# Kernel optimization log

Hardware: AMD Instinct MI355X
Metric: run time of the kernel (lower is better)

## Reference

```python
import jax, jax.numpy as jnp
import numpy as np

DIM = 256
NUM_EXPERTS = 16
EXPERT_HIDDEN = 128
ROUTER_HIDDEN = 64
N_TOKENS = 32768


def setup_inputs() -> dict:
    key = jax.random.key(0)
    ks = jax.random.split(key, 9)
    s = lambda fan_in: 1.0 / np.sqrt(fan_in)
    x = jax.random.normal(ks[0], (N_TOKENS, DIM), dtype=jnp.float32)
    # Router params (Linear(DIM,64) -> ReLU -> Linear(64,E))
    r_w1 = jax.random.uniform(ks[1], (DIM, ROUTER_HIDDEN), jnp.float32, -s(DIM), s(DIM))
    r_b1 = jax.random.uniform(ks[2], (ROUTER_HIDDEN,), jnp.float32, -s(DIM), s(DIM))
    r_w2 = jax.random.uniform(ks[3], (ROUTER_HIDDEN, NUM_EXPERTS), jnp.float32, -s(ROUTER_HIDDEN), s(ROUTER_HIDDEN))
    r_b2 = jax.random.uniform(ks[4], (NUM_EXPERTS,), jnp.float32, -s(ROUTER_HIDDEN), s(ROUTER_HIDDEN))
    # Expert params, stacked over experts: Linear(DIM,128) -> Tanh -> Linear(128,DIM)
    e_w1 = jax.random.uniform(ks[5], (NUM_EXPERTS, DIM, EXPERT_HIDDEN), jnp.float32, -s(DIM), s(DIM))
    e_b1 = jax.random.uniform(ks[6], (NUM_EXPERTS, EXPERT_HIDDEN), jnp.float32, -s(DIM), s(DIM))
    e_w2 = jax.random.uniform(ks[7], (NUM_EXPERTS, EXPERT_HIDDEN, DIM), jnp.float32, -s(EXPERT_HIDDEN), s(EXPERT_HIDDEN))
    e_b2 = jax.random.uniform(ks[8], (NUM_EXPERTS, DIM), jnp.float32, -s(EXPERT_HIDDEN), s(EXPERT_HIDDEN))
    return {"x": x, "r_w1": r_w1, "r_b1": r_b1, "r_w2": r_w2, "r_b2": r_b2,
            "e_w1": e_w1, "e_b1": e_b1, "e_w2": e_w2, "e_b2": e_b2}


def reference(x, r_w1, r_b1, r_w2, r_b2, e_w1, e_b1, e_w2, e_b2):
    # Router: softmax(Linear(ReLU(Linear(x)))), temp=1.0
    h_r = jax.nn.relu(x @ r_w1 + r_b1)                      # [N, 64]
    w = jax.nn.softmax(h_r @ r_w2 + r_b2, axis=-1)          # [N, E]
    # All experts densely (faithful to the reference loop), batched over E.
    h = jnp.tanh(jnp.einsum('nd,edh->neh', x, e_w1) + e_b1[None, :, :])   # [N, E, H]
    outs = jnp.einsum('neh,ehd->ned', h, e_w2) + e_b2[None, :, :]         # [N, E, D]
    # Top-2 gating: mask, renormalize, combine.
    top_val, top_idx = jax.lax.top_k(w, 2)                  # [N, 2]
    n = w.shape[0]
    mask = jnp.zeros_like(w).at[jnp.arange(n)[:, None], top_idx].set(1.0)
    w_top = w * mask
    w_top = w_top / (jnp.sum(w_top, axis=-1, keepdims=True) + 1e-8)
    y_pred = jnp.einsum('ne,ned->nd', w_top, outs)          # [N, D]
    return (y_pred, w)
```

## Files before the change

### kernel.cpp

```cpp
#include <hip/hip_runtime.h>
#include <math.h>

#define NT 32768
#define DIM 256
#define NE 16
#define EH 128
#define RH 64
#define TB 64

#define IB (NT * DIM)
#define WS_COUNTS (IB)
#define WS_OFFSETS (IB + 16)
#define WS_CURSORS (IB + 33)
#define WS_NBLK (IB + 49)
#define WS_TABLE (IB + 64)
#define WS_TOKE (IB + 4096)
#define WS_LIST (WS_TOKE + 2 * NT)
#define WS_TOKG (WS_LIST + 2 * NT)
#define WS_LIST_G (WS_TOKG + 2 * NT)
#define WS_END_I (WS_LIST_G + 2 * NT)
#define U_W1T (2 * WS_END_I)
#define U_W2T (U_W1T + NE * DIM * EH)
#define U_XG (U_W2T + NE * DIM * EH)

typedef __attribute__((ext_vector_type(4))) float f32x4;
typedef __attribute__((ext_vector_type(8))) short bf16x8;
typedef __attribute__((ext_vector_type(8))) unsigned short us8;

#define SWZ9(b) ((b) ^ (((b) >> 5) & 0x70))
#define SWZ8(b) ((b) ^ (((b) >> 4) & 0x70))

__device__ inline unsigned short f2bf(float f) {
    unsigned int bits = __builtin_bit_cast(unsigned int, f);
    bits += 0x7fffu + ((bits >> 16) & 1u);
    return (unsigned short)(bits >> 16);
}

__global__ __launch_bounds__(256) void router_kernel(
    const float* __restrict__ x,
    const float* __restrict__ rw1, const float* __restrict__ rb1,
    const float* __restrict__ rw2, const float* __restrict__ rb2,
    float* __restrict__ w_out, int* __restrict__ wsi, float* __restrict__ wsf)
{
    __shared__ float xT[64][68];
    __shared__ float w1s[64][64];
    __shared__ float hs[64][68];
    __shared__ float ls[64][20];
    __shared__ int scnt[16];

    const int tid = threadIdx.x;
    const int tok0 = blockIdx.x * 64;
    if (tid < 16) scnt[tid] = 0;

    float acc[4][4];
#pragma unroll
    for (int i = 0; i < 4; ++i)
#pragma unroll
        for (int j = 0; j < 4; ++j) acc[i][j] = 0.f;

    const int tt = (tid & 15) * 4;
    const int hh = (tid >> 4) * 4;

    for (int kc = 0; kc < 4; ++kc) {
        __syncthreads();
#pragma unroll
        for (int i = 0; i < 4; ++i) {
            int idx = tid + 256 * i;
            int t = idx >> 4;
            int d4 = (idx & 15) * 4;
            float4 v = *(const float4*)(x + (size_t)(tok0 + t) * DIM + kc * 64 + d4);
            xT[d4 + 0][t] = v.x; xT[d4 + 1][t] = v.y;
            xT[d4 + 2][t] = v.z; xT[d4 + 3][t] = v.w;
        }
#pragma unroll
        for (int i = 0; i < 4; ++i) {
            int idx = tid + 256 * i;
            int d = idx >> 4;
            int h4 = (idx & 15) * 4;
            *(float4*)&w1s[d][h4] = *(const float4*)(rw1 + (size_t)(kc * 64 + d) * RH + h4);
        }
        __syncthreads();
#pragma unroll 8
        for (int d = 0; d < 64; ++d) {
            const float4 xa4 = *(const float4*)&xT[d][tt];
            const float4 wv4 = *(const float4*)&w1s[d][hh];
            const float xa[4] = {xa4.x, xa4.y, xa4.z, xa4.w};
            const float wv[4] = {wv4.x, wv4.y, wv4.z, wv4.w};
#pragma unroll
            for (int i = 0; i < 4; ++i)
#pragma unroll
                for (int j = 0; j < 4; ++j)
                    acc[i][j] = fmaf(xa[i], wv[j], acc[i][j]);
        }
    }
    __syncthreads();
    {
        const float4 b4 = *(const float4*)(rb1 + hh);
        const float b[4] = {b4.x, b4.y, b4.z, b4.w};
#pragma unroll
        for (int i = 0; i < 4; ++i) {
            float4 hv;
            hv.x = fmaxf(acc[i][0] + b[0], 0.f);
            hv.y = fmaxf(acc[i][1] + b[1], 0.f);
            hv.z = fmaxf(acc[i][2] + b[2], 0.f);
            hv.w = fmaxf(acc[i][3] + b[3], 0.f);
            *(float4*)&hs[tt + i][hh] = hv;
        }
    }
    __syncthreads();
    {
        int tok = tid >> 2;
        int e0 = (tid & 3) * 4;
        float l[4] = {0.f, 0.f, 0.f, 0.f};
#pragma unroll 8
        for (int k = 0; k < 64; ++k) {
            float hv = hs[tok][k];
            float4 wv = *(const float4*)(rw2 + k * NE + e0);
            l[0] = fmaf(hv, wv.x, l[0]);
            l[1] = fmaf(hv, wv.y, l[1]);
            l[2] = fmaf(hv, wv.z, l[2]);
            l[3] = fmaf(hv, wv.w, l[3]);
        }
        float4 lb = *(const float4*)(rb2 + e0);
        ls[tok][e0 + 0] = l[0] + lb.x;
        ls[tok][e0 + 1] = l[1] + lb.y;
        ls[tok][e0 + 2] = l[2] + lb.z;
        ls[tok][e0 + 3] = l[3] + lb.w;
    }
    __syncthreads();
    if (tid < 64) {
        const int tok = tid;
        const int gt = tok0 + tok;
        float v[16];
        float m = -1e30f;
#pragma unroll
        for (int e = 0; e < 16; ++e) { v[e] = ls[tok][e]; m = fmaxf(m, v[e]); }
        float s = 0.f;
#pragma unroll
        for (int e = 0; e < 16; ++e) { v[e] = expf(v[e] - m); s += v[e]; }
        const float inv = 1.0f / s;
#pragma unroll
        for (int e = 0; e < 16; ++e) v[e] *= inv;
#pragma unroll
        for (int e = 0; e < 16; e += 4) {
            float4 wv = make_float4(v[e], v[e + 1], v[e + 2], v[e + 3]);
            *(float4*)(w_out + (size_t)gt * NE + e) = wv;
        }
        float v1 = -1.f, v2 = -1.f; int i1 = 0, i2 = 0;
#pragma unroll
        for (int e = 0; e < 16; ++e) {
            if (v[e] > v1) { v2 = v1; i2 = i1; v1 = v[e]; i1 = e; }
            else if (v[e] > v2) { v2 = v[e]; i2 = e; }
        }
        const float den = v1 + v2 + 1e-8f;
        atomicAdd(&scnt[i1], 1);
        atomicAdd(&scnt[i2], 1);
        wsi[WS_TOKE + 2 * gt + 0] = i1;
        wsi[WS_TOKE + 2 * gt + 1] = i2;
        wsf[WS_TOKG + 2 * gt + 0] = v1 / den;
        wsf[WS_TOKG + 2 * gt + 1] = v2 / den;
    }
    __syncthreads();
    if (tid < 16 && scnt[tid]) atomicAdd(&wsi[WS_COUNTS + tid], scnt[tid]);
}

__global__ __launch_bounds__(256) void wprep_kernel(
    const float* __restrict__ ew1, const float* __restrict__ ew2,
    unsigned short* __restrict__ w1t, unsigned short* __restrict__ w2t)
{
    __shared__ float t[64][65];
    int b = blockIdx.x;
    const float* src; unsigned short* dst; int R, C, tr, tc;
    if (b < 128) {
        int e = b >> 3, t8 = b & 7; tr = t8 >> 1; tc = t8 & 1;
        src = ew1 + (size_t)e * DIM * EH; R = DIM; C = EH;
        dst = w1t + (size_t)e * DIM * EH;
    } else {
        int b2 = b - 128; int e = b2 >> 3, t8 = b2 & 7; tr = t8 & 1; tc = t8 >> 1;
        src = ew2 + (size_t)e * EH * DIM; R = EH; C = DIM;
        dst = w2t + (size_t)e * EH * DIM;
    }
    const int R0 = tr * 64, C0 = tc * 64;
    const int tid = threadIdx.x;
#pragma unroll
    for (int q = 0; q < 4; ++q) {
        int r = (tid >> 4) + q * 16, c = (tid & 15) * 4;
        float4 v = *(const float4*)(src + (size_t)(R0 + r) * C + C0 + c);
        t[r][c] = v.x; t[r][c + 1] = v.y; t[r][c + 2] = v.z; t[r][c + 3] = v.w;
    }
    __syncthreads();
#pragma unroll
    for (int q = 0; q < 2; ++q) {
        int rp = (tid >> 3) + q * 32, c0 = (tid & 7) * 8;
        us8 u;
#pragma unroll
        for (int k = 0; k < 8; ++k) u[k] = f2bf(t[c0 + k][rp]);
        *(us8*)(dst + (size_t)(C0 + rp) * R + R0 + c0) = u;
    }
}

__global__ __launch_bounds__(64) void scan_kernel(int* __restrict__ wsi)
{
    __shared__ int soff[17], snc[16];
    const int tid = threadIdx.x;
    if (tid == 0) {
        int off = 0, nb = 0;
        soff[0] = 0;
        for (int e = 0; e < NE; ++e) {
            int c = wsi[WS_COUNTS + e];
            wsi[WS_CURSORS + e] = off;
            wsi[WS_OFFSETS + e] = off;
            off += c;
            soff[e + 1] = off;
            snc[e] = nb;
            nb += (c + TB - 1) / TB;
        }
        wsi[WS_OFFSETS + NE] = off;
        wsi[WS_NBLK] = nb;
    }
    __syncthreads();
    for (int e = 0; e < NE; ++e) {
        int nc = (soff[e + 1] - soff[e] + TB - 1) / TB;
        for (int k = tid; k < nc; k += 64)
            wsi[WS_TABLE + snc[e] + k] = (e << 16) | k;
    }
}

__global__ __launch_bounds__(256) void scatter_kernel(int* __restrict__ wsi, float* __restrict__ wsf)
{
    __shared__ int scnt[16], sbase[16];
    const int tid = threadIdx.x;
    const int t = blockIdx.x * 256 + tid;
    if (tid < 16) scnt[tid] = 0;
    __syncthreads();
    const int e0 = wsi[WS_TOKE + 2 * t + 0];
    const int e1 = wsi[WS_TOKE + 2 * t + 1];
    const int l0 = atomicAdd(&scnt[e0], 1);
    const int l1 = atomicAdd(&scnt[e1], 1);
    __syncthreads();
    if (tid < 16) sbase[tid] = scnt[tid] ? atomicAdd(&wsi[WS_CURSORS + tid], scnt[tid]) : 0;
    __syncthreads();
    const int p0 = sbase[e0] + l0;
    const int p1 = sbase[e1] + l1;
    wsi[WS_LIST + p0] = (t << 1);
    wsf[WS_LIST_G + p0] = wsf[WS_TOKG + 2 * t + 0];
    wsi[WS_LIST + p1] = (t << 1) | 1;
    wsf[WS_LIST_G + p1] = wsf[WS_TOKG + 2 * t + 1];
}

__global__ __launch_bounds__(256) void gather_kernel(
    const float* __restrict__ x, const int* __restrict__ wsi,
    unsigned short* __restrict__ xg)
{
    const int tid = threadIdx.x;
    const int p = blockIdx.x * 32 + (tid >> 3);
    const int sub = tid & 7;
    const int tok = wsi[WS_LIST + p] >> 1;
    const float* src = x + (size_t)tok * DIM + sub * 32;
    unsigned short* dst = xg + (size_t)p * DIM + sub * 32;
    float4 v[8];
#pragma unroll
    for (int i = 0; i < 8; ++i) v[i] = *(const float4*)(src + i * 4);
#pragma unroll
    for (int i = 0; i < 4; ++i) {
        us8 u;
        u[0] = f2bf(v[2 * i].x);     u[1] = f2bf(v[2 * i].y);
        u[2] = f2bf(v[2 * i].z);     u[3] = f2bf(v[2 * i].w);
        u[4] = f2bf(v[2 * i + 1].x); u[5] = f2bf(v[2 * i + 1].y);
        u[6] = f2bf(v[2 * i + 1].z); u[7] = f2bf(v[2 * i + 1].w);
        *(us8*)(dst + i * 8) = u;
    }
}

__global__ __launch_bounds__(256, 1) void expert_kernel(
    const unsigned short* __restrict__ xg,
    const float* __restrict__ eb1, const float* __restrict__ eb2,
    const unsigned short* __restrict__ w1t, const unsigned short* __restrict__ w2t,
    const int* __restrict__ wsi, const float* __restrict__ wsf,
    float* __restrict__ y, float* __restrict__ part1)
{
    __shared__ unsigned short smem[16384];
    if ((int)blockIdx.x >= wsi[WS_NBLK]) return;

    const int ent = wsi[WS_TABLE + blockIdx.x];
    const int e = ent >> 16;
    const int c = ent & 0xffff;
    const int start = wsi[WS_OFFSETS + e] + c * TB;
    const int cnt = min(TB, wsi[WS_OFFSETS + e + 1] - start);

    const int tid = threadIdx.x;
    const int lane = tid & 63, w = tid >> 6;
    const int l15 = lane & 15;
    const int kq = lane >> 4;
    const int q4 = kq * 4;
    char* lds = (char*)smem;

    const char* xrow = (const char*)(xg + (size_t)start * DIM);
    us8 ubuf[8];
#pragma unroll
    for (int i = 0; i < 8; ++i)
        ubuf[i] = *(const us8*)(xrow + (tid + i * 256) * 16);

    const char* w1e = (const char*)(w1t + (size_t)e * DIM * EH);
    bf16x8 b1[8][2];
#pragma unroll
    for (int ks = 0; ks < 8; ++ks)
#pragma unroll
        for (int nt = 0; nt < 2; ++nt)
            b1[ks][nt] = *(const bf16x8*)(w1e + (w * 32 + nt * 16 + l15) * 512 + ks * 64 + kq * 16);

#pragma unroll
    for (int i = 0; i < 8; ++i)
        *(us8*)(lds + SWZ9((tid + i * 256) * 16)) = ubuf[i];
    __syncthreads();

    f32x4 zero4; zero4[0] = zero4[1] = zero4[2] = zero4[3] = 0.f;
    f32x4 acc[4][2];
#pragma unroll
    for (int i = 0; i < 4; ++i)
#pragma unroll
        for (int j = 0; j < 2; ++j) acc[i][j] = zero4;

#pragma unroll
    for (int ks = 0; ks < 8; ++ks) {
        bf16x8 a[4];
#pragma unroll
        for (int mt = 0; mt < 4; ++mt)
            a[mt] = *(const bf16x8*)(lds + SWZ9((mt * 16 + l15) * 512 + ks * 64 + kq * 16));
#pragma unroll
        for (int mt = 0; mt < 4; ++mt)
#pragma unroll
            for (int nt = 0; nt < 2; ++nt)
                acc[mt][nt] = __builtin_amdgcn_mfma_f32_16x16x32_bf16(a[mt], b1[ks][nt], acc[mt][nt], 0, 0, 0);
    }

    const char* w2e = (const char*)(w2t + (size_t)e * EH * DIM);
    bf16x8 b2a[4][2];
#pragma unroll
    for (int ks = 0; ks < 4; ++ks)
#pragma unroll
        for (int nt = 0; nt < 2; ++nt)
            b2a[ks][nt] = *(const bf16x8*)(w2e + (w * 64 + nt * 16 + l15) * 256 + ks * 64 + kq * 16);

    __syncthreads();

#pragma unroll
    for (int nt = 0; nt < 2; ++nt) {
        const int h = w * 32 + nt * 16 + l15;
        const float b1v = eb1[e * EH + h];
#pragma unroll
        for (int mt = 0; mt < 4; ++mt)
#pragma unroll
            for (int r = 0; r < 4; ++r) {
                int tok = mt * 16 + q4 + r;
                *(unsigned short*)(lds + SWZ8(tok * 256 + h * 2)) = f2bf(tanhf(acc[mt][nt][r] + b1v));
            }
    }
    __syncthreads();

    bf16x8 b2b[4][2];
#pragma unroll
    for (int ks = 0; ks < 4; ++ks)
#pragma unroll
        for (int nt = 0; nt < 2; ++nt)
            b2b[ks][nt] = *(const bf16x8*)(w2e + (w * 64 + 32 + nt * 16 + l15) * 256 + ks * 64 + kq * 16);

    {
        f32x4 acc2[4][2];
#pragma unroll
        for (int i = 0; i < 4; ++i)
#pragma unroll
            for (int j = 0; j < 2; ++j) acc2[i][j] = zero4;
#pragma unroll
        for (int ks = 0; ks < 4; ++ks) {
            bf16x8 a[4];
#pragma unroll
            for (int mt = 0; mt < 4; ++mt)
                a[mt] = *(const bf16x8*)(lds + SWZ8((mt * 16 + l15) * 256 + ks * 64 + kq * 16));
#pragma unroll
            for (int mt = 0; mt < 4; ++mt)
#pragma unroll
                for (int nt = 0; nt < 2; ++nt)
                    acc2[mt][nt] = __builtin_amdgcn_mfma_f32_16x16x32_bf16(a[mt], b2a[ks][nt], acc2[mt][nt], 0, 0, 0);
        }
        float b2v[2];
#pragma unroll
        for (int nt = 0; nt < 2; ++nt)
            b2v[nt] = eb2[e * DIM + w * 64 + nt * 16 + l15];
#pragma unroll
        for (int mt = 0; mt < 4; ++mt)
#pragma unroll
            for (int r = 0; r < 4; ++r) {
                int rl = mt * 16 + q4 + r;
                if (rl < cnt) {
                    int entry = wsi[WS_LIST + start + rl];
                    int tok = entry >> 1;
                    float g = wsf[WS_LIST_G + start + rl];
                    float* dst = ((entry & 1) ? part1 : y) + (size_t)tok * DIM + w * 64;
#pragma unroll
                    for (int nt = 0; nt < 2; ++nt)
                        dst[nt * 16 + l15] = g * (acc2[mt][nt][r] + b2v[nt]);
                }
            }
    }
    {
        f32x4 acc2[4][2];
#pragma unroll
        for (int i = 0; i < 4; ++i)
#pragma unroll
            for (int j = 0; j < 2; ++j) acc2[i][j] = zero4;
#pragma unroll
        for (int ks = 0; ks < 4; ++ks) {
            bf16x8 a[4];
#pragma unroll
            for (int mt = 0; mt < 4; ++mt)
                a[mt] = *(const bf16x8*)(lds + SWZ8((mt * 16 + l15) * 256 + ks * 64 + kq * 16));
#pragma unroll
            for (int mt = 0; mt < 4; ++mt)
#pragma unroll
                for (int nt = 0; nt < 2; ++nt)
                    acc2[mt][nt] = __builtin_amdgcn_mfma_f32_16x16x32_bf16(a[mt], b2b[ks][nt], acc2[mt][nt], 0, 0, 0);
        }
        float b2v[2];
#pragma unroll
        for (int nt = 0; nt < 2; ++nt)
            b2v[nt] = eb2[e * DIM + w * 64 + 32 + nt * 16 + l15];
#pragma unroll
        for (int mt = 0; mt < 4; ++mt)
#pragma unroll
            for (int r = 0; r < 4; ++r) {
                int rl = mt * 16 + q4 + r;
                if (rl < cnt) {
                    int entry = wsi[WS_LIST + start + rl];
                    int tok = entry >> 1;
                    float g = wsf[WS_LIST_G + start + rl];
                    float* dst = ((entry & 1) ? part1 : y) + (size_t)tok * DIM + w * 64 + 32;
#pragma unroll
                    for (int nt = 0; nt < 2; ++nt)
                        dst[nt * 16 + l15] = g * (acc2[mt][nt][r] + b2v[nt]);
                }
            }
    }
}

__global__ __launch_bounds__(256) void combine_kernel(float* __restrict__ y,
                                                      const float* __restrict__ part1)
{
    const size_t i = ((size_t)blockIdx.x * 256 + threadIdx.x) * 4;
    float4 a = *(float4*)(y + i);
    const float4 b = *(const float4*)(part1 + i);
    a.x += b.x; a.y += b.y; a.z += b.z; a.w += b.w;
    *(float4*)(y + i) = a;
}

extern "C" void kernel_launch(void* const* d_in, const int* in_sizes, int n_in,
                              void* d_out, int out_size, void* d_ws, size_t ws_size,
                              hipStream_t stream)
{
    const float* x = (const float*)d_in[0];
    const float* rw1 = (const float*)d_in[1];
    const float* rb1 = (const float*)d_in[2];
    const float* rw2 = (const float*)d_in[3];
    const float* rb2 = (const float*)d_in[4];
    const float* ew1 = (const float*)d_in[5];
    const float* eb1 = (const float*)d_in[6];
    const float* ew2 = (const float*)d_in[7];
    const float* eb2 = (const float*)d_in[8];

    float* y = (float*)d_out;
    float* w_out = y + (size_t)NT * DIM;
    int* wsi = (int*)d_ws;
    float* wsf = (float*)d_ws;
    float* part1 = (float*)d_ws;
    unsigned short* wsu = (unsigned short*)d_ws;

    hipMemsetAsync(wsi + WS_COUNTS, 0, NE * sizeof(int), stream);

    wprep_kernel<<<256, 256, 0, stream>>>(ew1, ew2, wsu + U_W1T, wsu + U_W2T);
    router_kernel<<<NT / 64, 256, 0, stream>>>(x, rw1, rb1, rw2, rb2, w_out, wsi, wsf);
    scan_kernel<<<1, 64, 0, stream>>>(wsi);
    scatter_kernel<<<NT / 256, 256, 0, stream>>>(wsi, wsf);
    gather_kernel<<<2 * NT / 32, 256, 0, stream>>>(x, wsi, wsu + U_XG);
    expert_kernel<<<2 * NT / TB + NE, 256, 0, stream>>>(wsu + U_XG, eb1, eb2,
                                                        wsu + U_W1T, wsu + U_W2T,
                                                        wsi, wsf, y, part1);
    combine_kernel<<<NT * DIM / 1024, 256, 0, stream>>>(y, part1);
}
```

Before: 137.7 us.

## Make expert kernel persistent with 2 blocks/CU, LDS-cached routing, fast tanh

Turns the expert kernel into a persistent grid of 512 blocks that loop over the block table, instead of launching one block per tile. It raises the launch bound to two blocks per CU, stages each tile's token list and gate values in shared memory once, and replaces tanhf with an exp-based fast tanh. The aim is to cut launch and early-exit overhead, improve latency hiding, and remove repeated global reads of the routing lists. The tradeoff is tighter register pressure and possible spills, plus an extra barrier per tile and small tanh accuracy changes.

```diff
diff --git a/kernel.cpp b/kernel.cpp
--- a/kernel.cpp
+++ b/kernel.cpp
@@ -7,6 +7,7 @@
 #define EH 128
 #define RH 64
 #define TB 64
+#define NPERS 512
 
 #define IB (NT * DIM)
 #define WS_COUNTS (IB)
@@ -36,6 +37,12 @@
     return (unsigned short)(bits >> 16);
 }
 
+__device__ inline float fast_tanh(float v) {
+    float cv = fminf(fmaxf(v, -15.f), 15.f);
+    float ex = __expf(2.f * cv);
+    return (ex - 1.f) / (ex + 1.f);
+}
+
 __global__ __launch_bounds__(256) void router_kernel(
     const float* __restrict__ x,
     const float* __restrict__ rw1, const float* __restrict__ rb1,
@@ -272,7 +279,7 @@
     }
 }
 
-__global__ __launch_bounds__(256, 1) void expert_kernel(
+__global__ __launch_bounds__(256, 2) void expert_kernel(
     const unsigned short* __restrict__ xg,
     const float* __restrict__ eb1, const float* __restrict__ eb2,
     const unsigned short* __restrict__ w1t, const unsigned short* __restrict__ w2t,
@@ -280,166 +287,175 @@
     float* __restrict__ y, float* __restrict__ part1)
 {
     __shared__ unsigned short smem[16384];
-    if ((int)blockIdx.x >= wsi[WS_NBLK]) return;
-
-    const int ent = wsi[WS_TABLE + blockIdx.x];
-    const int e = ent >> 16;
-    const int c = ent & 0xffff;
-    const int start = wsi[WS_OFFSETS + e] + c * TB;
-    const int cnt = min(TB, wsi[WS_OFFSETS + e + 1] - start);
-
+    __shared__ int sl[64];
+    __shared__ float sg[64];
+
+    const int nblk = wsi[WS_NBLK];
     const int tid = threadIdx.x;
     const int lane = tid & 63, w = tid >> 6;
     const int l15 = lane & 15;
     const int kq = lane >> 4;
     const int q4 = kq * 4;
     char* lds = (char*)smem;
-
-    const char* xrow = (const char*)(xg + (size_t)start * DIM);
-    us8 ubuf[8];
-#pragma unroll
-    for (int i = 0; i < 8; ++i)
-        ubuf[i] = *(const us8*)(xrow + (tid + i * 256) * 16);
-
-    const char* w1e = (const char*)(w1t + (size_t)e * DIM * EH);
-    bf16x8 b1[8][2];
-#pragma unroll
-    for (int ks = 0; ks < 8; ++ks)
-#pragma unroll
-        for (int nt = 0; nt < 2; ++nt)
-            b1[ks][nt] = *(const bf16x8*)(w1e + (w * 32 + nt * 16 + l15) * 512 + ks * 64 + kq * 16);
-
-#pragma unroll
-    for (int i = 0; i < 8; ++i)
-        *(us8*)(lds + SWZ9((tid + i * 256) * 16)) = ubuf[i];
-    __syncthreads();
-
     f32x4 zero4; zero4[0] = zero4[1] = zero4[2] = zero4[3] = 0.f;
-    f32x4 acc[4][2];
-#pragma unroll
-    for (int i = 0; i < 4; ++i)
-#pragma unroll
-        for (int j = 0; j < 2; ++j) acc[i][j] = zero4;
-
-#pragma unroll
-    for (int ks = 0; ks < 8; ++ks) {
-        bf16x8 a[4];
-#pragma unroll
-        for (int mt = 0; mt < 4; ++mt)
-            a[mt] = *(const bf16x8*)(lds + SWZ9((mt * 16 + l15) * 512 + ks * 64 + kq * 16));
-#pragma unroll
-        for (int mt = 0; mt < 4; ++mt)
+
+    for (int bi = blockIdx.x; bi < nblk; bi += NPERS) {
+        const int ent = wsi[WS_TABLE + bi];
+        const int e = ent >> 16;
+        const int c = ent & 0xffff;
+        const int start = wsi[WS_OFFSETS + e] + c * TB;
+        const int cnt = min(TB, wsi[WS_OFFSETS + e + 1] - start);
+
+        __syncthreads();
+
+        const char* xrow = (const char*)(xg + (size_t)start * DIM);
+        us8 ubuf[8];
+#pragma unroll
+        for (int i = 0; i < 8; ++i)
+            ubuf[i] = *(const us8*)(xrow + (tid + i * 256) * 16);
+
+        const char* w1e = (const char*)(w1t + (size_t)e * DIM * EH);
+        bf16x8 b1[8][2];
+#pragma unroll
+        for (int ks = 0; ks < 8; ++ks)
 #pragma unroll
             for (int nt = 0; nt < 2; ++nt)
-                acc[mt][nt] = __builtin_amdgcn_mfma_f32_16x16x32_bf16(a[mt], b1[ks][nt], acc[mt][nt], 0, 0, 0);
-    }
-
-    const char* w2e = (const char*)(w2t + (size_t)e * EH * DIM);
-    bf16x8 b2a[4][2];
-#pragma unroll
-    for (int ks = 0; ks < 4; ++ks)
-#pragma unroll
-        for (int nt = 0; nt < 2; ++nt)
-            b2a[ks][nt] = *(const bf16x8*)(w2e + (w * 64 + nt * 16 + l15) * 256 + ks * 64 + kq * 16);
-
-    __syncthreads();
-
-#pragma unroll
-    for (int nt = 0; nt < 2; ++nt) {
-        const int h = w * 32 + nt * 16 + l15;
-        const float b1v = eb1[e * EH + h];
-#pragma unroll
-        for (int mt = 0; mt < 4; ++mt)
-#pragma unroll
-            for (int r = 0; r < 4; ++r) {
-                int tok = mt * 16 + q4 + r;
-                *(unsigned short*)(lds + SWZ8(tok * 256 + h * 2)) = f2bf(tanhf(acc[mt][nt][r] + b1v));
+                b1[ks][nt] = *(const bf16x8*)(w1e + (w * 32 + nt * 16 + l15) * 512 + ks * 64 + kq * 16);
+
+        if (tid < 64) {
+            sl[tid] = (tid < cnt) ? wsi[WS_LIST + start + tid] : 0;
+            sg[tid] = (tid < cnt) ? wsf[WS_LIST_G + start + tid] : 0.f;
+        }
+
+#pragma unroll
+        for (int i = 0; i < 8; ++i)
+            *(us8*)(lds + SWZ9((tid + i * 256) * 16)) = ubuf[i];
+        __syncthreads();
+
+        f32x4 acc[4][2];
+#pragma unroll
+        for (int i = 0; i < 4; ++i)
+#pragma unroll
+            for (int j = 0; j < 2; ++j) acc[i][j] = zero4;
+
+#pragma unroll
+        for (int ks = 0; ks < 8; ++ks) {
+            bf16x8 a[4];
+#pragma unroll
+            for (int mt = 0; mt < 4; ++mt)
+                a[mt] = *(const bf16x8*)(lds + SWZ9((mt * 16 + l15) * 512 + ks * 64 + kq * 16));
+#pragma unroll
+            for (int mt = 0; mt < 4; ++mt)
+#pragma unroll
+                for (int nt = 0; nt < 2; ++nt)
+                    acc[mt][nt] = __builtin_amdgcn_mfma_f32_16x16x32_bf16(a[mt], b1[ks][nt], acc[mt][nt], 0, 0, 0);
+        }
+
+        const char* w2e = (const char*)(w2t + (size_t)e * EH * DIM);
+        bf16x8 b2a[4][2];
+#pragma unroll
+        for (int ks = 0; ks < 4; ++ks)
+#pragma unroll
+            for (int nt = 0; nt < 2; ++nt)
+                b2a[ks][nt] = *(const bf16x8*)(w2e + (w * 64 + nt * 16 + l15) * 256 + ks * 64 + kq * 16);
+
+        __syncthreads();
+
+#pragma unroll
+        for (int nt = 0; nt < 2; ++nt) {
+            const int h = w * 32 + nt * 16 + l15;
+            const float b1v = eb1[e * EH + h];
+#pragma unroll
+            for (int mt = 0; mt < 4; ++mt)
+#pragma unroll
+                for (int r = 0; r < 4; ++r) {
+                    int tok = mt * 16 + q4 + r;
+                    *(unsigned short*)(lds + SWZ8(tok * 256 + h * 2)) = f2bf(fast_tanh(acc[mt][nt][r] + b1v));
+                }
+        }
+        __syncthreads();
+
+        bf16x8 b2b[4][2];
+#pragma unroll
+        for (int ks = 0; ks < 4; ++ks)
+#pragma unroll
+            for (int nt = 0; nt < 2; ++nt)
+                b2b[ks][nt] = *(const bf16x8*)(w2e + (w * 64 + 32 + nt * 16 + l15) * 256 + ks * 64 + kq * 16);
+
+        {
+            f32x4 acc2[4][2];
+#pragma unroll
+            for (int i = 0; i < 4; ++i)
+#pragma unroll
+                for (int j = 0; j < 2; ++j) acc2[i][j] = zero4;
+#pragma unroll
+            for (int ks = 0; ks < 4; ++ks) {
+                bf16x8 a[4];
+#pragma unroll
+                for (int mt = 0; mt < 4; ++mt)
+                    a[mt] = *(const bf16x8*)(lds + SWZ8((mt * 16 + l15) * 256 + ks * 64 + kq * 16));
+#pragma unroll
+                for (int mt = 0; mt < 4; ++mt)
+#pragma unroll
+                    for (int nt = 0; nt < 2; ++nt)
+                        acc2[mt][nt] = __builtin_amdgcn_mfma_f32_16x16x32_bf16(a[mt], b2a[ks][nt], acc2[mt][nt], 0, 0, 0);
             }
-    }
-    __syncthreads();
-
-    bf16x8 b2b[4][2];
-#pragma unroll
-    for (int ks = 0; ks < 4; ++ks)
-#pragma unroll
-        for (int nt = 0; nt < 2; ++nt)
-            b2b[ks][nt] = *(const bf16x8*)(w2e + (w * 64 + 32 + nt * 16 + l15) * 256 + ks * 64 + kq * 16);
-
-    {
-        f32x4 acc2[4][2];
-#pragma unroll
-        for (int i = 0; i < 4; ++i)
-#pragma unroll
-            for (int j = 0; j < 2; ++j) acc2[i][j] = zero4;
-#pragma unroll
-        for (int ks = 0; ks < 4; ++ks) {
-            bf16x8 a[4];
+            float b2v[2];
+#pragma unroll
+            for (int nt = 0; nt < 2; ++nt)
+                b2v[nt] = eb2[e * DIM + w * 64 + nt * 16 + l15];
 #pragma unroll
             for (int mt = 0; mt < 4; ++mt)
-                a[mt] = *(const bf16x8*)(lds + SWZ8((mt * 16 + l15) * 256 + ks * 64 + kq * 16));
+#pragma unroll
+                for (int r = 0; r < 4; ++r) {
+                    int rl = mt * 16 + q4 + r;
+                    if (rl < cnt) {
+                        int entry = sl[rl];
+                        float g = sg[rl];
+                        float* dst = ((entry & 1) ? part1 : y) + (size_t)(entry >> 1) * DIM + w * 64;
+#pragma unroll
+                        for (int nt = 0; nt < 2; ++nt)
+                            dst[nt * 16 + l15] = g * (acc2[mt][nt][r] + b2v[nt]);
+                    }
+                }
+        }
+        {
+            f32x4 acc2[4][2];
+#pragma unroll
+            for (int i = 0; i < 4; ++i)
+#pragma unroll
+                for (int j = 0; j < 2; ++j) acc2[i][j] = zero4;
+#pragma unroll
+            for (int ks = 0; ks < 4; ++ks) {
+                bf16x8 a[4];
+#pragma unroll
+                for (int mt = 0; mt < 4; ++mt)
+                    a[mt] = *(const bf16x8*)(lds + SWZ8((mt * 16 + l15) * 256 + ks * 64 + kq * 16));
+#pragma unroll
+                for (int mt = 0; mt < 4; ++mt)
+#pragma unroll
+                    for (int nt = 0; nt < 2; ++nt)
+                        acc2[mt][nt] = __builtin_amdgcn_mfma_f32_16x16x32_bf16(a[mt], b2b[ks][nt], acc2[mt][nt], 0, 0, 0);
+            }
+            float b2v[2];
+#pragma unroll
+            for (int nt = 0; nt < 2; ++nt)
+                b2v[nt] = eb2[e * DIM + w * 64 + 32 + nt * 16 + l15];
 #pragma unroll
             for (int mt = 0; mt < 4; ++mt)
 #pragma unroll
-                for (int nt = 0; nt < 2; ++nt)
-                    acc2[mt][nt] = __builtin_amdgcn_mfma_f32_16x16x32_bf16(a[mt], b2a[ks][nt], acc2[mt][nt], 0, 0, 0);
-        }
-        float b2v[2];
-#pragma unroll
-        for (int nt = 0; nt < 2; ++nt)
-            b2v[nt] = eb2[e * DIM + w * 64 + nt * 16 + l15];
-#pragma unroll
-        for (int mt = 0; mt < 4; ++mt)
-#pragma unroll
-            for (int r = 0; r < 4; ++r) {
-                int rl = mt * 16 + q4 + r;
-                if (rl < cnt) {
-                    int entry = wsi[WS_LIST + start + rl];
-                    int tok = entry >> 1;
-                    float g = wsf[WS_LIST_G + start + rl];
-                    float* dst = ((entry & 1) ? part1 : y) + (size_t)tok * DIM + w * 64;
-#pragma unroll
-                    for (int nt = 0; nt < 2; ++nt)
-                        dst[nt * 16 + l15] = g * (acc2[mt][nt][r] + b2v[nt]);
+                for (int r = 0; r < 4; ++r) {
+                    int rl = mt * 16 + q4 + r;
+                    if (rl < cnt) {
+                        int entry = sl[rl];
+                        float g = sg[rl];
+                        float* dst = ((entry & 1) ? part1 : y) + (size_t)(entry >> 1) * DIM + w * 64 + 32;
+#pragma unroll
+                        for (int nt = 0; nt < 2; ++nt)
+                            dst[nt * 16 + l15] = g * (acc2[mt][nt][r] + b2v[nt]);
+                    }
                 }
-            }
-    }
-    {
-        f32x4 acc2[4][2];
-#pragma unroll
-        for (int i = 0; i < 4; ++i)
-#pragma unroll
-            for (int j = 0; j < 2; ++j) acc2[i][j] = zero4;
-#pragma unroll
-        for (int ks = 0; ks < 4; ++ks) {
-            bf16x8 a[4];
-#pragma unroll
-            for (int mt = 0; mt < 4; ++mt)
-                a[mt] = *(const bf16x8*)(lds + SWZ8((mt * 16 + l15) * 256 + ks * 64 + kq * 16));
-#pragma unroll
-            for (int mt = 0; mt < 4; ++mt)
-#pragma unroll
-                for (int nt = 0; nt < 2; ++nt)
-                    acc2[mt][nt] = __builtin_amdgcn_mfma_f32_16x16x32_bf16(a[mt], b2b[ks][nt], acc2[mt][nt], 0, 0, 0);
-        }
-        float b2v[2];
-#pragma unroll
-        for (int nt = 0; nt < 2; ++nt)
-            b2v[nt] = eb2[e * DIM + w * 64 + 32 + nt * 16 + l15];
-#pragma unroll
-        for (int mt = 0; mt < 4; ++mt)
-#pragma unroll
-            for (int r = 0; r < 4; ++r) {
-                int rl = mt * 16 + q4 + r;
-                if (rl < cnt) {
-                    int entry = wsi[WS_LIST + start + rl];
-                    int tok = entry >> 1;
-                    float g = wsf[WS_LIST_G + start + rl];
-                    float* dst = ((entry & 1) ? part1 : y) + (size_t)tok * DIM + w * 64 + 32;
-#pragma unroll
-                    for (int nt = 0; nt < 2; ++nt)
-                        dst[nt * 16 + l15] = g * (acc2[mt][nt][r] + b2v[nt]);
-                }
-            }
+        }
     }
 }
 
@@ -481,8 +497,8 @@
     scan_kernel<<<1, 64, 0, stream>>>(wsi);
     scatter_kernel<<<NT / 256, 256, 0, stream>>>(wsi, wsf);
     gather_kernel<<<2 * NT / 32, 256, 0, stream>>>(x, wsi, wsu + U_XG);
-    expert_kernel<<<2 * NT / TB + NE, 256, 0, stream>>>(wsu + U_XG, eb1, eb2,
-                                                        wsu + U_W1T, wsu + U_W2T,
-                                                        wsi, wsf, y, part1);
+    expert_kernel<<<NPERS, 256, 0, stream>>>(wsu + U_XG, eb1, eb2,
+                                             wsu + U_W1T, wsu + U_W2T,
+                                             wsi, wsf, y, part1);
     combine_kernel<<<NT * DIM / 1024, 256, 0, stream>>>(y, part1);
 }
```

After: 138.4 us. No clear change (+0.5%).
